# Performance work log

Measured on AMD Instinct MI355X. Metric: run time of the kernel, lower is better.

Reference implementation:

```python
import jax, jax.numpy as jnp
import numpy as np
from jax import lax

EPS = 1e-5
DIM = 96      # channels = dim
KS = 96       # kernel_size == H == W
GROUPS = 8
BATCH = 4
FFN_F = 2.66

# relative index table: emb[c, i, j] = rel[c, i - j + KS - 1]
_REL_IDX = (np.arange(KS)[:, None] - np.arange(KS)[None, :] + KS - 1).reshape(-1)


def _bn(x, g, b, ax):
    """BatchNorm (training-mode batch statistics) over all axes except `ax`."""
    axes = tuple(i for i in range(x.ndim) if i != ax)
    m = x.mean(axes, keepdims=True)
    v = x.var(axes, keepdims=True)
    sh = [1] * x.ndim
    sh[ax] = -1
    return (x - m) / jnp.sqrt(v + EPS) * g.reshape(sh) + b.reshape(sh)


def _ln(x, w, b):
    """WithBias LayerNorm over channel dim of NCHW (per-pixel over C)."""
    m = x.mean(1, keepdims=True)
    v = x.var(1, keepdims=True)
    return (x - m) / jnp.sqrt(v + EPS) * w[None, :, None, None] + b[None, :, None, None]


def _axial(x, wqkv, gq, bq, rel, gs, bs, go, bo, width):
    # x: (N, C, H, W)
    xp = x.transpose(0, 2, 1, 3) if width else x.transpose(0, 3, 1, 2)
    N, Wd, C, L = xp.shape
    gp = C // GROUPS  # group_planes
    xb = xp.reshape(N * Wd, C, L)
    qkv = _bn(jnp.einsum('oc,bcl->bol', wqkv, xb), gq, bq, 1)
    qkv = qkv.reshape(N * Wd, GROUPS, 2 * gp, L)
    q, k, v = qkv[:, :, :gp // 2], qkv[:, :, gp // 2:gp], qkv[:, :, gp:]
    emb = rel[:, _REL_IDX].reshape(2 * gp, L, L)
    qe, ke, ve = emb[:gp // 2], emb[gp // 2:gp], emb[gp:]
    qk = jnp.einsum('bgci,bgcj->bgij', q, k)
    qr = jnp.einsum('bgci,cij->bgij', q, qe)
    kr = jnp.einsum('bgci,cij->bgij', k, ke).transpose(0, 1, 3, 2)
    sim = _bn(jnp.concatenate([qk, qr, kr], 1), gs, bs, 1)
    sim = sim.reshape(N * Wd, 3, GROUPS, L, L).sum(1)
    sim = jax.nn.softmax(sim, axis=3)
    sv = jnp.einsum('bgij,bgcj->bgci', sim, v)
    sve = jnp.einsum('bgij,cij->bgci', sim, ve)
    out = _bn(jnp.concatenate([sv, sve], -1).reshape(N * Wd, 2 * C, L), go, bo, 1)
    out = out.reshape(N, Wd, C, 2, L).sum(3)
    return out.transpose(0, 2, 1, 3) if width else out.transpose(0, 2, 3, 1)


def _ffn(x, win, wdw, wout):
    h = jnp.einsum('oc,bchw->bohw', win, x)
    h = lax.conv_general_dilated(h, wdw, (1, 1), 'SAME',
                                 dimension_numbers=('NCHW', 'OIHW', 'NCHW'),
                                 feature_group_count=h.shape[1])
    x1, x2 = jnp.split(h, 2, axis=1)
    return jnp.einsum('oc,bchw->bohw', wout, jax.nn.gelu(x1, approximate=False) * x2)


def setup_inputs() -> dict:
    key = jax.random.key(0)
    ks = jax.random.split(key, 8)
    dim, gp = DIM, DIM // GROUPS
    hid = int(dim * FFN_F)
    f = jax.random.normal
    d = {'x': f(ks[0], (BATCH, dim, KS, KS), jnp.float32)}
    d['ln1_w'] = jnp.ones(dim); d['ln1_b'] = jnp.zeros(dim)
    for p, i in (('h_', 1), ('w_', 2)):
        k1, k2 = jax.random.split(ks[i])
        d[p + 'wqkv'] = f(k1, (2 * dim, dim), jnp.float32) * float(np.sqrt(1.0 / dim))
        d[p + 'gqkv'] = jnp.ones(2 * dim); d[p + 'bqkv'] = jnp.zeros(2 * dim)
        d[p + 'rel'] = f(k2, (2 * gp, 2 * KS - 1), jnp.float32) * float(np.sqrt(1.0 / gp))
        d[p + 'gsim'] = jnp.ones(3 * GROUPS); d[p + 'bsim'] = jnp.zeros(3 * GROUPS)
        d[p + 'gout'] = jnp.ones(2 * dim); d[p + 'bout'] = jnp.zeros(2 * dim)
    d['ln2_w'] = jnp.ones(dim); d['ln2_b'] = jnp.zeros(dim)
    d['ffn_win'] = f(ks[3], (2 * hid, dim), jnp.float32) * float(np.sqrt(1.0 / dim))
    d['ffn_wdw'] = f(ks[4], (2 * hid, 1, 3, 3), jnp.float32) * 0.1
    d['ffn_wout'] = f(ks[5], (dim, hid), jnp.float32) * float(np.sqrt(1.0 / hid))
    return d


def reference(x, ln1_w, ln1_b,
              h_wqkv, h_gqkv, h_bqkv, h_rel, h_gsim, h_bsim, h_gout, h_bout,
              w_wqkv, w_gqkv, w_bqkv, w_rel, w_gsim, w_bsim, w_gout, w_bout,
              ln2_w, ln2_b, ffn_win, ffn_wdw, ffn_wout):
    y = _ln(x, ln1_w, ln1_b)
    y = _axial(y, h_wqkv, h_gqkv, h_bqkv, h_rel, h_gsim, h_bsim, h_gout, h_bout, False)
    y = _axial(y, w_wqkv, w_gqkv, w_bqkv, w_rel, w_gsim, w_bsim, w_gout, w_bout, True)
    x = x + y
    x = x + _ffn(_ln(x, ln2_w, ln2_b), ffn_win, ffn_wdw, ffn_wout)
    return x
```

## Files before the change

kernel.cpp:

```cpp
#include <hip/hip_runtime.h>
#include <hip/hip_bf16.h>
#include <math.h>

using bf16 = __hip_bfloat16;

#define NB 4
#define C_ 96
#define NPIX 36864
#define IMG 9216
#define CH_ST 9216
#define N_ST 884736
#define HID 255
#define EPSF 1e-5f
#define TOT 3538944

__global__ __launch_bounds__(256) void ln_kernel(const float* __restrict__ X,
                                                 float* __restrict__ Y,
                                                 const float* __restrict__ w,
                                                 const float* __restrict__ b) {
  int pix = blockIdx.x * 256 + threadIdx.x;
  if (pix >= NPIX) return;
  int n = pix / IMG, p = pix % IMG;
  const float* xp = X + (long)n * N_ST + p;
  float s = 0.f, sq = 0.f;
  for (int c = 0; c < C_; c++) { float v = xp[c * CH_ST]; s += v; sq += v * v; }
  float m = s * (1.f / C_);
  float var = fmaxf(sq * (1.f / C_) - m * m, 0.f);
  float r = rsqrtf(var + EPSF);
  float* yp = Y + (long)n * N_ST + p;
  for (int c = 0; c < C_; c++)
    yp[c * CH_ST] = (xp[c * CH_ST] - m) * r * w[c] + b[c];
}

__global__ void trans_kernel(const float* __restrict__ Y0, float* __restrict__ Y0C) {
  __shared__ float T[32][33];
  int nc = blockIdx.z; int n = nc / C_, c = nc % C_;
  int h0 = blockIdx.x * 32, w0 = blockIdx.y * 32;
  int tx = threadIdx.x, ty = threadIdx.y;
  const float* src = Y0 + (long)n * N_ST + (long)c * CH_ST;
  for (int r = 0; r < 4; r++)
    T[ty + 8 * r][tx] = src[(h0 + ty + 8 * r) * 96 + w0 + tx];
  __syncthreads();
  float* dst = Y0C + (long)c * NPIX + (long)n * IMG;
  for (int r = 0; r < 4; r++)
    dst[(w0 + ty + 8 * r) * 96 + h0 + tx] = T[tx][ty + 8 * r];
}

template<int TM, int TN, int EPI>
__global__ __launch_bounds__(256) void gemm_kernel(
    const float* __restrict__ A, const float* __restrict__ B,
    float* __restrict__ Cout, int M, int K, int NperZ,
    long bCstride, long bZstride, int batch,
    const float* __restrict__ X1, float* __restrict__ OutF) {
  constexpr int NT = TN / 16;
  constexpr int RT = TM / 16;
  __shared__ float As[32][TM];
  __shared__ float Bs[32][TN + 4];
  const int tx = threadIdx.x, ty = threadIdx.y;
  const int tid = ty * 16 + tx;
  const int m0 = blockIdx.y * TM;
  const int q0 = blockIdx.x * TN;
  const int z  = blockIdx.z;
  const float* Bz = B + (long)z * bZstride;
  float acc[RT][NT];
  #pragma unroll
  for (int a = 0; a < RT; a++)
    #pragma unroll
    for (int b = 0; b < NT; b++) acc[a][b] = 0.f;

  for (int kk = 0; kk < K; kk += 32) {
    #pragma unroll
    for (int it = 0; it < (32 * TM) / 256; it++) {
      int i = tid + it * 256;
      int c = i / TM, r = i % TM;
      int mm = m0 + r, kc = kk + c;
      As[c][r] = (mm < M && kc < K) ? A[(long)mm * K + kc] : 0.f;
    }
    #pragma unroll
    for (int it = 0; it < (32 * TN) / 256; it++) {
      int i = tid + it * 256;
      int c = i / TN, q = i % TN;
      int kc = kk + c;
      Bs[c][q] = (kc < K) ? Bz[(long)kc * bCstride + q0 + q] : 0.f;
    }
    __syncthreads();
    for (int kc = 0; kc < 32; kc++) {
      float av[RT];
      if constexpr (RT % 4 == 0) {
        #pragma unroll
        for (int u = 0; u < RT / 4; u++) {
          float4 a4 = *(const float4*)&As[kc][ty * RT + 4 * u];
          av[4 * u] = a4.x; av[4 * u + 1] = a4.y; av[4 * u + 2] = a4.z; av[4 * u + 3] = a4.w;
        }
      } else {
        #pragma unroll
        for (int u = 0; u < RT / 2; u++) {
          float2 a2 = *(const float2*)&As[kc][ty * RT + 2 * u];
          av[2 * u] = a2.x; av[2 * u + 1] = a2.y;
        }
      }
      float bv[NT];
      #pragma unroll
      for (int v4 = 0; v4 < NT / 4; v4++) {
        float4 b4 = *(const float4*)&Bs[kc][v4 * 64 + tx * 4];
        bv[v4 * 4] = b4.x; bv[v4 * 4 + 1] = b4.y; bv[v4 * 4 + 2] = b4.z; bv[v4 * 4 + 3] = b4.w;
      }
      #pragma unroll
      for (int a = 0; a < RT; a++)
        #pragma unroll
        for (int b = 0; b < NT; b++)
          acc[a][b] = fmaf(av[a], bv[b], acc[a][b]);
    }
    __syncthreads();
  }
  const long oStride = (long)NperZ * gridDim.z;
  if (EPI == 0) {
    #pragma unroll
    for (int a = 0; a < RT; a++) {
      int mm = m0 + ty * RT + a;
      if (mm < M) {
        float* dst = Cout + (long)mm * oStride + (long)z * NperZ + q0;
        #pragma unroll
        for (int v4 = 0; v4 < NT / 4; v4++)
          *(float4*)(dst + v4 * 64 + tx * 4) =
              make_float4(acc[a][v4 * 4], acc[a][v4 * 4 + 1],
                          acc[a][v4 * 4 + 2], acc[a][v4 * 4 + 3]);
      }
    }
  } else {
    #pragma unroll
    for (int a = 0; a < RT; a++) {
      int mm = m0 + ty * RT + a;
      if (mm < M) {
        #pragma unroll
        for (int v4 = 0; v4 < NT / 4; v4++) {
          int Q = q0 + v4 * 64 + tx * 4;
          int n = batch + z + Q / IMG, p = Q % IMG;
          long base = (long)n * N_ST + (long)mm * CH_ST + p;
          #pragma unroll
          for (int b = 0; b < 4; b++)
            OutF[base + b] = acc[a][v4 * 4 + b] + X1[base + b];
        }
      }
    }
  }
}

__global__ __launch_bounds__(1024) void rowstat_kernel(const float* __restrict__ D,
                                                       const float* __restrict__ g,
                                                       const float* __restrict__ b,
                                                       float2* __restrict__ aff) {
  int o = blockIdx.x;
  const float4* p = (const float4*)(D + (long)o * NPIX);
  float s = 0.f, sq = 0.f;
  for (int i = threadIdx.x; i < NPIX / 4; i += 1024) {
    float4 v = p[i];
    s  += v.x + v.y + v.z + v.w;
    sq += v.x * v.x + v.y * v.y + v.z * v.z + v.w * v.w;
  }
  for (int off = 32; off; off >>= 1) { s += __shfl_down(s, off); sq += __shfl_down(sq, off); }
  __shared__ float ss[16], ssq[16];
  int wv = threadIdx.x >> 6, lane = threadIdx.x & 63;
  if (lane == 0) { ss[wv] = s; ssq[wv] = sq; }
  __syncthreads();
  if (threadIdx.x == 0) {
    float S = 0.f, SQ = 0.f;
    #pragma unroll
    for (int i = 0; i < 16; i++) { S += ss[i]; SQ += ssq[i]; }
    float m = S / (float)NPIX;
    float var = fmaxf(SQ / (float)NPIX - m * m, 0.f);
    float sc = g[o] * rsqrtf(var + EPSF);
    aff[o] = make_float2(sc, b[o] - m * sc);
  }
}

__global__ void relstat_kernel(const float* __restrict__ relp, float* __restrict__ tbl) {
  int i = threadIdx.x;
  if (i >= 96) return;
  int side = blockIdx.x / 27, row = blockIdx.x % 27;
  const float* base = relp + side * 6 * 191;
  float* T = tbl + side * 27 * 96;
  if (row < 6) {
    float s = 0.f;
    for (int d = 0; d < 96; d++) s += base[row * 191 + i + d];
    T[row * 96 + i] = s;
  } else {
    int p = row - 6, c = 0;
    while (p >= 6 - c) { p -= 6 - c; c++; }
    int c2 = c + p;
    float s = 0.f;
    for (int d = 0; d < 96; d++) s += base[c * 191 + i + d] * base[c2 * 191 + i + d];
    T[576 + (row - 6) * 96 + i] = s;
  }
}

__global__ __launch_bounds__(256) void simstat2_kernel(const float* __restrict__ QKV,
                                                       const float2* __restrict__ aff,
                                                       const float* __restrict__ tbl,
                                                       float* __restrict__ stats) {
  int g = blockIdx.x & 7, chunk = blockIdx.x >> 3;
  int bbg = threadIdx.x >> 5, lane = threadIdx.x & 31;
  int bb = chunk * 8 + bbg;
  const float* Aq = tbl;
  const float* Wq = tbl + 6 * 96;
  const float* Ak = tbl + 27 * 96;
  const float* Wk = tbl + 27 * 96 + 6 * 96;
  float Sq[6] = {}, Sk[6] = {}, Gq[21] = {}, Gk[21] = {};
  float lq = 0.f, lsq = 0.f, lk = 0.f, lsk = 0.f;
  #pragma unroll
  for (int ii = 0; ii < 3; ii++) {
    int i = lane + 32 * ii;
    float qv[6], kv[6];
    #pragma unroll
    for (int c = 0; c < 6; c++) {
      int oq = g * 24 + c, ok = g * 24 + 6 + c;
      float2 a = aff[oq], b2 = aff[ok];
      qv[c] = QKV[(long)oq * NPIX + bb * 96 + i] * a.x + a.y;
      kv[c] = QKV[(long)ok * NPIX + bb * 96 + i] * b2.x + b2.y;
      Sq[c] += qv[c]; Sk[c] += kv[c];
      lq = fmaf(qv[c], Aq[c * 96 + i], lq);
      lk = fmaf(kv[c], Ak[c * 96 + i], lk);
    }
    int p = 0;
    #pragma unroll
    for (int c = 0; c < 6; c++)
      #pragma unroll
      for (int c2 = c; c2 < 6; c2++, p++) {
        float f = (c == c2) ? 1.f : 2.f;
        float pq = qv[c] * qv[c2], pk = kv[c] * kv[c2];
        Gq[p] += pq; Gk[p] += pk;
        lsq = fmaf(pq * f, Wq[p * 96 + i], lsq);
        lsk = fmaf(pk * f, Wk[p * 96 + i], lsk);
      }
  }
  #pragma unroll
  for (int off = 16; off; off >>= 1) {
    #pragma unroll
    for (int c = 0; c < 6; c++) { Sq[c] += __shfl_down(Sq[c], off, 32); Sk[c] += __shfl_down(Sk[c], off, 32); }
    #pragma unroll
    for (int p = 0; p < 21; p++) { Gq[p] += __shfl_down(Gq[p], off, 32); Gk[p] += __shfl_down(Gk[p], off, 32); }
    lq += __shfl_down(lq, off, 32);  lsq += __shfl_down(lsq, off, 32);
    lk += __shfl_down(lk, off, 32);  lsk += __shfl_down(lsk, off, 32);
  }
  __shared__ float red[6];
  if (threadIdx.x < 6) red[threadIdx.x] = 0.f;
  __syncthreads();
  if (lane == 0) {
    float sqk = 0.f, sqk2 = 0.f;
    #pragma unroll
    for (int c = 0; c < 6; c++) sqk += Sq[c] * Sk[c];
    int p = 0;
    #pragma unroll
    for (int c = 0; c < 6; c++)
      #pragma unroll
      for (int c2 = c; c2 < 6; c2++, p++)
        sqk2 += ((c == c2) ? 1.f : 2.f) * Gq[p] * Gk[p];
    atomicAdd(&red[0], sqk); atomicAdd(&red[3], sqk2);
    atomicAdd(&red[1], lq);  atomicAdd(&red[4], lsq);
    atomicAdd(&red[2], lk);  atomicAdd(&red[5], lsk);
  }
  __syncthreads();
  if (threadIdx.x < 3) {
    atomicAdd(&stats[(threadIdx.x * 8 + g) * 2 + 0], red[threadIdx.x]);
    atomicAdd(&stats[(threadIdx.x * 8 + g) * 2 + 1], red[threadIdx.x + 3]);
  }
}

__global__ void simfin_kernel(const float* __restrict__ stats,
                              const float* __restrict__ gsim,
                              float* __restrict__ scale) {
  int t = threadIdx.x;
  if (t < 24) {
    float cnt = 384.f * 9216.f;
    float m = stats[t * 2] / cnt;
    float var = fmaxf(stats[t * 2 + 1] / cnt - m * m, 0.f);
    scale[t] = gsim[t] * rsqrtf(var + EPSF);
  }
}

__global__ __launch_bounds__(256) void attn_kernel(const float* __restrict__ QKV,
                                                   const float2* __restrict__ aff,
                                                   const float* __restrict__ relp,
                                                   const float* __restrict__ sscale,
                                                   float* __restrict__ OutPre) {
  int blk = blockIdx.x;
  int bb = blk / 24, rem = blk % 24;
  int g = rem / 3, iq = rem % 3;
  int i0 = iq * 32;
  __shared__ float qI[6][32];
  __shared__ float kF[6][96];
  __shared__ float vF[12][96];
  __shared__ float rl[24][191];
  __shared__ float P[32][100];
  __shared__ float rinv[32];
  int tid = threadIdx.x;
  float s0 = sscale[g], s1 = sscale[8 + g], s2 = sscale[16 + g];
  for (int i = tid; i < 6 * 32; i += 256) {
    int c = i >> 5, l = i & 31;
    int o = g * 24 + c; float2 a = aff[o];
    qI[c][l] = QKV[(long)o * NPIX + bb * 96 + i0 + l] * a.x + a.y;
  }
  for (int i = tid; i < 6 * 96; i += 256) {
    int c = i / 96, l = i % 96;
    int o = g * 24 + 6 + c; float2 a = aff[o];
    kF[c][l] = QKV[(long)o * NPIX + bb * 96 + l] * a.x + a.y;
  }
  for (int i = tid; i < 12 * 96; i += 256) {
    int c = i / 96, l = i % 96;
    int o = g * 24 + 12 + c; float2 a = aff[o];
    vF[c][l] = QKV[(long)o * NPIX + bb * 96 + l] * a.x + a.y;
  }
  for (int i = tid; i < 24 * 191; i += 256) {
    int r = i / 191;
    float sc = (r < 6) ? s1 : ((r < 12) ? s2 : 1.f);
    (&rl[0][0])[i] = relp[i] * sc;
  }
  __syncthreads();
  int hw = tid >> 5, l32 = tid & 31;
  {
    int til = hw * 4;
    int ti = i0 + til;
    int tj = l32 * 3;
    int d0 = ti - tj + 93;
    int e0 = tj - ti + 92;
    float ap[4][3] = {};
    #pragma unroll
    for (int c = 0; c < 6; c++) {
      float4 q4 = *(const float4*)&qI[c][til];
      float qv[4] = {q4.x, q4.y, q4.z, q4.w};
      float kv[3], kv0[3], rq[6], rk[6];
      #pragma unroll
      for (int j = 0; j < 3; j++) { kv[j] = kF[c][tj + j]; kv0[j] = s0 * kv[j]; }
      #pragma unroll
      for (int u = 0; u < 6; u++) { rq[u] = rl[c][d0 + u]; rk[u] = rl[6 + c][e0 + u]; }
      #pragma unroll
      for (int ii = 0; ii < 4; ii++)
        #pragma unroll
        for (int jj = 0; jj < 3; jj++) {
          ap[ii][jj] = fmaf(qv[ii], kv0[jj], ap[ii][jj]);
          ap[ii][jj] = fmaf(qv[ii], rq[ii - jj + 2], ap[ii][jj]);
          ap[ii][jj] = fmaf(kv[jj], rk[jj - ii + 3], ap[ii][jj]);
        }
    }
    #pragma unroll
    for (int ii = 0; ii < 4; ii++)
      #pragma unroll
      for (int jj = 0; jj < 3; jj++)
        P[til + ii][l32 * 3 + jj] = ap[ii][jj];
  }
  __syncthreads();
  for (int r = hw; r < 32; r += 8) {
    float v0 = P[r][l32], v1 = P[r][l32 + 32], v2 = P[r][l32 + 64];
    float mx = fmaxf(v0, fmaxf(v1, v2));
    #pragma unroll
    for (int off = 16; off; off >>= 1) mx = fmaxf(mx, __shfl_xor(mx, off, 32));
    float e0 = __expf(v0 - mx), e1 = __expf(v1 - mx), e2 = __expf(v2 - mx);
    P[r][l32] = e0; P[r][l32 + 32] = e1; P[r][l32 + 64] = e2;
    float s = e0 + e1 + e2;
    #pragma unroll
    for (int off = 16; off; off >>= 1) s += __shfl_xor(s, off, 32);
    if (l32 == 0) rinv[r] = 1.f / s;
  }
  __syncthreads();
  {
    int orr0 = hw * 3;
    float acc3[3] = {};
    for (int jq = 0; jq < 24; jq++) {
      int j0 = jq * 4;
      float4 pv = *(const float4*)&P[l32][j0];
      #pragma unroll
      for (int u = 0; u < 3; u++) {
        int orr = orr0 + u, cc = orr >> 1;
        if ((orr & 1) == 0) {
          float4 vv = *(const float4*)&vF[cc][j0];
          acc3[u] += pv.x * vv.x + pv.y * vv.y + pv.z * vv.z + pv.w * vv.w;
        } else {
          const float* rv = rl[12 + cc];
          int bse = (i0 + l32) - j0 + 92;
          float f0 = rv[bse], f1 = rv[bse + 1], f2 = rv[bse + 2], f3 = rv[bse + 3];
          acc3[u] += pv.w * f0 + pv.z * f1 + pv.y * f2 + pv.x * f3;
        }
      }
    }
    #pragma unroll
    for (int u = 0; u < 3; u++)
      OutPre[(long)(g * 24 + orr0 + u) * NPIX + bb * 96 + i0 + l32] = acc3[u] * rinv[l32];
  }
}

__global__ void apply1_kernel(const float* __restrict__ OutPre,
                              const float2* __restrict__ aff,
                              float* __restrict__ Y1) {
  __shared__ float T[32][33];
  int z = blockIdx.z; int n = z / C_, cf = z % C_;
  int h0 = blockIdx.x * 32, w0 = blockIdx.y * 32;
  int tx = threadIdx.x, ty = threadIdx.y;
  float2 a0 = aff[2 * cf], a1 = aff[2 * cf + 1];
  const float* r0 = OutPre + (long)(2 * cf) * NPIX + (long)n * IMG;
  const float* r1 = OutPre + (long)(2 * cf + 1) * NPIX + (long)n * IMG;
  for (int r = 0; r < 4; r++) {
    int w = w0 + ty + 8 * r;
    int idx = w * 96 + h0 + tx;
    T[ty + 8 * r][tx] = (r0[idx] * a0.x + a0.y) + (r1[idx] * a1.x + a1.y);
  }
  __syncthreads();
  float* dst = Y1 + (long)n * N_ST + (long)cf * CH_ST;
  for (int r = 0; r < 4; r++)
    dst[(h0 + ty + 8 * r) * 96 + w0 + tx] = T[tx][ty + 8 * r];
}

__global__ __launch_bounds__(256) void apply2_kernel(const float* __restrict__ OutPre,
                                                     const float2* __restrict__ aff,
                                                     const float* __restrict__ X,
                                                     float* __restrict__ X1out) {
  int idx = blockIdx.x * 256 + threadIdx.x;
  if (idx >= TOT) return;
  int n = idx / N_ST;
  int rem = idx % N_ST;
  int cf = rem / CH_ST;
  int p = rem % CH_ST;
  long off = (long)n * IMG + p;
  float2 a0 = aff[2 * cf], a1 = aff[2 * cf + 1];
  float v = OutPre[(long)(2 * cf) * NPIX + off] * a0.x + a0.y
          + OutPre[(long)(2 * cf + 1) * NPIX + off] * a1.x + a1.y
          + X[idx];
  X1out[idx] = v;
}

__global__ __launch_bounds__(256) void dwglu_kernel(const float* __restrict__ H,
                                                    const float* __restrict__ Wdw,
                                                    float* __restrict__ Gout) {
  int idx = blockIdx.x * 256 + threadIdx.x;
  if (idx >= HID * IMG) return;
  int c = idx / IMG;
  int p = idx % IMG, y = p / 96, x = p % 96;
  const float* h1 = H + (long)c * IMG;
  const float* h2 = H + (long)(c + HID) * IMG;
  const float* w1 = Wdw + c * 9;
  const float* w2 = Wdw + (c + HID) * 9;
  float acc1 = 0.f, acc2 = 0.f;
  #pragma unroll
  for (int dy = -1; dy <= 1; dy++) {
    int yy = y + dy; if (yy < 0 || yy >= 96) continue;
    #pragma unroll
    for (int dx = -1; dx <= 1; dx++) {
      int xx = x + dx; if (xx < 0 || xx >= 96) continue;
      int wi = (dy + 1) * 3 + dx + 1;
      acc1 = fmaf(h1[yy * 96 + xx], w1[wi], acc1);
      acc2 = fmaf(h2[yy * 96 + xx], w2[wi], acc2);
    }
  }
  float ge = 0.5f * acc1 * (1.f + erff(acc1 * 0.70710678118654752f));
  Gout[idx] = ge * acc2;
}

extern "C" void kernel_launch(void* const* d_in, const int* in_sizes, int n_in,
                              void* d_out, int out_size, void* d_ws, size_t ws_size,
                              hipStream_t stream) {
  const float* x       = (const float*)d_in[0];
  const float* ln1w    = (const float*)d_in[1];
  const float* ln1b    = (const float*)d_in[2];
  const float* h_wqkv  = (const float*)d_in[3];
  const float* h_gqkv  = (const float*)d_in[4];
  const float* h_bqkv  = (const float*)d_in[5];
  const float* h_rel   = (const float*)d_in[6];
  const float* h_gsim  = (const float*)d_in[7];
  const float* h_gout  = (const float*)d_in[9];
  const float* h_bout  = (const float*)d_in[10];
  const float* w_wqkv  = (const float*)d_in[11];
  const float* w_gqkv  = (const float*)d_in[12];
  const float* w_bqkv  = (const float*)d_in[13];
  const float* w_rel   = (const float*)d_in[14];
  const float* w_gsim  = (const float*)d_in[15];
  const float* w_gout  = (const float*)d_in[17];
  const float* w_bout  = (const float*)d_in[18];
  const float* ln2w    = (const float*)d_in[19];
  const float* ln2b    = (const float*)d_in[20];
  const float* ffn_win = (const float*)d_in[21];
  const float* ffn_wdw = (const float*)d_in[22];
  const float* ffn_wout= (const float*)d_in[23];
  float* out = (float*)d_out;

  float* ws = (float*)d_ws;
  float* P = ws;
  float* Q = ws + 3538944;
  float* R = ws + 7077888;
  float* S = ws + 14155776;
  float* Gall = R;
  float* Hbuf = ws + 16478208;
  float* stats = ws + 21233664;
  const size_t need_bytes = (21233664ull + 8192ull) * 4ull;
  if (ws_size < need_bytes) return;

  float2* qkv_aff = (float2*)stats;
  float2* out_aff = (float2*)(stats + 384);
  float*  sim_st  = stats + 768;
  float*  sim_sc  = stats + 864;
  float*  tbl     = stats + 1024;

  hipMemsetAsync(sim_st, 0, 96 * sizeof(float), stream);

  dim3 b256(256), b1616(16, 16), b328(32, 8);

  ln_kernel<<<144, b256, 0, stream>>>(x, P, ln1w, ln1b);
  trans_kernel<<<dim3(3, 3, 384), b328, 0, stream>>>(P, Q);

  gemm_kernel<96, 128, 0><<<dim3(288, 2, 1), b1616, 0, stream>>>(h_wqkv, Q, R,
      192, 96, 36864, 36864L, 0L, 0, nullptr, nullptr);
  rowstat_kernel<<<192, 1024, 0, stream>>>(R, h_gqkv, h_bqkv, qkv_aff);
  relstat_kernel<<<54, 96, 0, stream>>>(h_rel, tbl);
  simstat2_kernel<<<384, b256, 0, stream>>>(R, qkv_aff, tbl, sim_st);
  simfin_kernel<<<1, 32, 0, stream>>>(sim_st, h_gsim, sim_sc);
  attn_kernel<<<9216, b256, 0, stream>>>(R, qkv_aff, h_rel, sim_sc, S);
  rowstat_kernel<<<192, 1024, 0, stream>>>(S, h_gout, h_bout, out_aff);
  apply1_kernel<<<dim3(3, 3, 384), b328, 0, stream>>>(S, out_aff, P);

  gemm_kernel<96, 128, 0><<<dim3(72, 2, 4), b1616, 0, stream>>>(w_wqkv, P, R,
      192, 96, 9216, 9216L, 884736L, 0, nullptr, nullptr);
  rowstat_kernel<<<192, 1024, 0, stream>>>(R, w_gqkv, w_bqkv, qkv_aff);
  relstat_kernel<<<54, 96, 0, stream>>>(w_rel, tbl);
  simstat2_kernel<<<384, b256, 0, stream>>>(R, qkv_aff, tbl, sim_st + 48);
  simfin_kernel<<<1, 32, 0, stream>>>(sim_st + 48, w_gsim, sim_sc + 24);
  attn_kernel<<<9216, b256, 0, stream>>>(R, qkv_aff, w_rel, sim_sc + 24, S);
  rowstat_kernel<<<192, 1024, 0, stream>>>(S, w_gout, w_bout, out_aff);
  apply2_kernel<<<13824, b256, 0, stream>>>(S, out_aff, x, P);

  ln_kernel<<<144, b256, 0, stream>>>(P, Q, ln2w, ln2b);
  for (int n = 0; n < NB; n++) {
    gemm_kernel<128, 64, 0><<<dim3(144, 4, 1), b1616, 0, stream>>>(ffn_win, Q + (long)n * N_ST, Hbuf,
        510, 96, 9216, 9216L, 0L, 0, nullptr, nullptr);
    dwglu_kernel<<<9180, b256, 0, stream>>>(Hbuf, ffn_wdw, Gall + (long)n * 2350080);
  }
  gemm_kernel<96, 64, 1><<<dim3(144, 1, 4), b1616, 0, stream>>>(ffn_wout, Gall, nullptr,
      96, 255, 9216, 9216L, 2350080L, 0, P, out);
}
```

Baseline: 941.7 us.

## Process all query tiles per block in axial attention to reuse staged K/V/rel

Each attention block now handles one (batch-row, group) pair and loops over the three 32-row query tiles, so the K, V and scaled relative-embedding tables are loaded into shared memory once instead of three times. The global loads of Q/K/V and the rel table are also vectorised to float4. The grid shrinks threefold, which cuts redundant staging traffic but leaves fewer blocks for latency hiding and adds extra barriers inside the loop.

```diff
diff --git a/kernel.cpp b/kernel.cpp
--- a/kernel.cpp
+++ b/kernel.cpp
@@ -284,107 +284,118 @@
                                                    const float* __restrict__ sscale,
                                                    float* __restrict__ OutPre) {
   int blk = blockIdx.x;
-  int bb = blk / 24, rem = blk % 24;
-  int g = rem / 3, iq = rem % 3;
-  int i0 = iq * 32;
-  __shared__ float qI[6][32];
+  int bb = blk >> 3, g = blk & 7;
+  __shared__ float qF[6][96];
   __shared__ float kF[6][96];
   __shared__ float vF[12][96];
-  __shared__ float rl[24][191];
+  __shared__ float rl[24 * 191];
   __shared__ float P[32][100];
-  __shared__ float rinv[32];
   int tid = threadIdx.x;
   float s0 = sscale[g], s1 = sscale[8 + g], s2 = sscale[16 + g];
-  for (int i = tid; i < 6 * 32; i += 256) {
-    int c = i >> 5, l = i & 31;
-    int o = g * 24 + c; float2 a = aff[o];
-    qI[c][l] = QKV[(long)o * NPIX + bb * 96 + i0 + l] * a.x + a.y;
-  }
-  for (int i = tid; i < 6 * 96; i += 256) {
-    int c = i / 96, l = i % 96;
-    int o = g * 24 + 6 + c; float2 a = aff[o];
-    kF[c][l] = QKV[(long)o * NPIX + bb * 96 + l] * a.x + a.y;
-  }
-  for (int i = tid; i < 12 * 96; i += 256) {
-    int c = i / 96, l = i % 96;
-    int o = g * 24 + 12 + c; float2 a = aff[o];
-    vF[c][l] = QKV[(long)o * NPIX + bb * 96 + l] * a.x + a.y;
-  }
-  for (int i = tid; i < 24 * 191; i += 256) {
-    int r = i / 191;
-    float sc = (r < 6) ? s1 : ((r < 12) ? s2 : 1.f);
-    (&rl[0][0])[i] = relp[i] * sc;
+  for (int i = tid; i < 288; i += 256) {
+    int half = i / 144, r = i % 144;
+    int c = r / 24, qd = r % 24;
+    int o = g * 24 + half * 6 + c;
+    float2 a = aff[o];
+    float4 v = *(const float4*)(QKV + (long)o * NPIX + bb * 96 + qd * 4);
+    float4 w = make_float4(v.x * a.x + a.y, v.y * a.x + a.y,
+                           v.z * a.x + a.y, v.w * a.x + a.y);
+    if (half == 0) *(float4*)&qF[c][qd * 4] = w;
+    else           *(float4*)&kF[c][qd * 4] = w;
+  }
+  for (int i = tid; i < 288; i += 256) {
+    int c = i / 24, qd = i % 24;
+    int o = g * 24 + 12 + c;
+    float2 a = aff[o];
+    float4 v = *(const float4*)(QKV + (long)o * NPIX + bb * 96 + qd * 4);
+    *(float4*)&vF[c][qd * 4] = make_float4(v.x * a.x + a.y, v.y * a.x + a.y,
+                                           v.z * a.x + a.y, v.w * a.x + a.y);
+  }
+  for (int i = tid; i < 1146; i += 256) {
+    int e = i * 4;
+    float4 v = *(const float4*)(relp + e);
+    float4 w;
+    w.x = v.x * ((e + 0) < 1146 ? s1 : (e + 0) < 2292 ? s2 : 1.f);
+    w.y = v.y * ((e + 1) < 1146 ? s1 : (e + 1) < 2292 ? s2 : 1.f);
+    w.z = v.z * ((e + 2) < 1146 ? s1 : (e + 2) < 2292 ? s2 : 1.f);
+    w.w = v.w * ((e + 3) < 1146 ? s1 : (e + 3) < 2292 ? s2 : 1.f);
+    *(float4*)&rl[e] = w;
   }
   __syncthreads();
   int hw = tid >> 5, l32 = tid & 31;
-  {
-    int til = hw * 4;
-    int ti = i0 + til;
-    int tj = l32 * 3;
-    int d0 = ti - tj + 93;
-    int e0 = tj - ti + 92;
-    float ap[4][3] = {};
-    #pragma unroll
-    for (int c = 0; c < 6; c++) {
-      float4 q4 = *(const float4*)&qI[c][til];
-      float qv[4] = {q4.x, q4.y, q4.z, q4.w};
-      float kv[3], kv0[3], rq[6], rk[6];
-      #pragma unroll
-      for (int j = 0; j < 3; j++) { kv[j] = kF[c][tj + j]; kv0[j] = s0 * kv[j]; }
-      #pragma unroll
-      for (int u = 0; u < 6; u++) { rq[u] = rl[c][d0 + u]; rk[u] = rl[6 + c][e0 + u]; }
+  for (int iq = 0; iq < 3; iq++) {
+    int i0 = iq * 32;
+    {
+      int til = hw * 4;
+      int ti = i0 + til;
+      int tj = l32 * 3;
+      int d0 = ti - tj + 93;
+      int e0 = tj - ti + 92;
+      float ap[4][3] = {};
+      #pragma unroll
+      for (int c = 0; c < 6; c++) {
+        float4 q4 = *(const float4*)&qF[c][ti];
+        float qv[4] = {q4.x, q4.y, q4.z, q4.w};
+        float kv[3], kv0[3], rq[6], rk[6];
+        #pragma unroll
+        for (int j = 0; j < 3; j++) { kv[j] = kF[c][tj + j]; kv0[j] = s0 * kv[j]; }
+        #pragma unroll
+        for (int u = 0; u < 6; u++) { rq[u] = rl[c * 191 + d0 + u]; rk[u] = rl[(6 + c) * 191 + e0 + u]; }
+        #pragma unroll
+        for (int ii = 0; ii < 4; ii++)
+          #pragma unroll
+          for (int jj = 0; jj < 3; jj++) {
+            ap[ii][jj] = fmaf(qv[ii], kv0[jj], ap[ii][jj]);
+            ap[ii][jj] = fmaf(qv[ii], rq[ii - jj + 2], ap[ii][jj]);
+            ap[ii][jj] = fmaf(kv[jj], rk[jj - ii + 3], ap[ii][jj]);
+          }
+      }
       #pragma unroll
       for (int ii = 0; ii < 4; ii++)
         #pragma unroll
-        for (int jj = 0; jj < 3; jj++) {
-          ap[ii][jj] = fmaf(qv[ii], kv0[jj], ap[ii][jj]);
-          ap[ii][jj] = fmaf(qv[ii], rq[ii - jj + 2], ap[ii][jj]);
-          ap[ii][jj] = fmaf(kv[jj], rk[jj - ii + 3], ap[ii][jj]);
+        for (int jj = 0; jj < 3; jj++)
+          P[til + ii][l32 * 3 + jj] = ap[ii][jj];
+    }
+    __syncthreads();
+    for (int r = hw; r < 32; r += 8) {
+      float v0 = P[r][l32], v1 = P[r][l32 + 32], v2 = P[r][l32 + 64];
+      float mx = fmaxf(v0, fmaxf(v1, v2));
+      #pragma unroll
+      for (int off = 16; off; off >>= 1) mx = fmaxf(mx, __shfl_xor(mx, off, 32));
+      float e0 = __expf(v0 - mx), e1 = __expf(v1 - mx), e2 = __expf(v2 - mx);
+      P[r][l32] = e0; P[r][l32 + 32] = e1; P[r][l32 + 64] = e2;
+      float s = e0 + e1 + e2;
+      #pragma unroll
+      for (int off = 16; off; off >>= 1) s += __shfl_xor(s, off, 32);
+      if (l32 == 0) P[r][96] = 1.f / s;
+    }
+    __syncthreads();
+    {
+      int orr0 = hw * 3;
+      float acc3[3] = {};
+      for (int jq = 0; jq < 24; jq++) {
+        int j0 = jq * 4;
+        float4 pv = *(const float4*)&P[l32][j0];
+        #pragma unroll
+        for (int u = 0; u < 3; u++) {
+          int orr = orr0 + u, cc = orr >> 1;
+          if ((orr & 1) == 0) {
+            float4 vv = *(const float4*)&vF[cc][j0];
+            acc3[u] += pv.x * vv.x + pv.y * vv.y + pv.z * vv.z + pv.w * vv.w;
+          } else {
+            const float* rv = &rl[(12 + cc) * 191];
+            int bse = (i0 + l32) - j0 + 92;
+            float f0 = rv[bse], f1 = rv[bse + 1], f2 = rv[bse + 2], f3 = rv[bse + 3];
+            acc3[u] += pv.w * f0 + pv.z * f1 + pv.y * f2 + pv.x * f3;
+          }
         }
-    }
-    #pragma unroll
-    for (int ii = 0; ii < 4; ii++)
-      #pragma unroll
-      for (int jj = 0; jj < 3; jj++)
-        P[til + ii][l32 * 3 + jj] = ap[ii][jj];
-  }
-  __syncthreads();
-  for (int r = hw; r < 32; r += 8) {
-    float v0 = P[r][l32], v1 = P[r][l32 + 32], v2 = P[r][l32 + 64];
-    float mx = fmaxf(v0, fmaxf(v1, v2));
-    #pragma unroll
-    for (int off = 16; off; off >>= 1) mx = fmaxf(mx, __shfl_xor(mx, off, 32));
-    float e0 = __expf(v0 - mx), e1 = __expf(v1 - mx), e2 = __expf(v2 - mx);
-    P[r][l32] = e0; P[r][l32 + 32] = e1; P[r][l32 + 64] = e2;
-    float s = e0 + e1 + e2;
-    #pragma unroll
-    for (int off = 16; off; off >>= 1) s += __shfl_xor(s, off, 32);
-    if (l32 == 0) rinv[r] = 1.f / s;
-  }
-  __syncthreads();
-  {
-    int orr0 = hw * 3;
-    float acc3[3] = {};
-    for (int jq = 0; jq < 24; jq++) {
-      int j0 = jq * 4;
-      float4 pv = *(const float4*)&P[l32][j0];
-      #pragma unroll
-      for (int u = 0; u < 3; u++) {
-        int orr = orr0 + u, cc = orr >> 1;
-        if ((orr & 1) == 0) {
-          float4 vv = *(const float4*)&vF[cc][j0];
-          acc3[u] += pv.x * vv.x + pv.y * vv.y + pv.z * vv.z + pv.w * vv.w;
-        } else {
-          const float* rv = rl[12 + cc];
-          int bse = (i0 + l32) - j0 + 92;
-          float f0 = rv[bse], f1 = rv[bse + 1], f2 = rv[bse + 2], f3 = rv[bse + 3];
-          acc3[u] += pv.w * f0 + pv.z * f1 + pv.y * f2 + pv.x * f3;
-        }
-      }
-    }
-    #pragma unroll
-    for (int u = 0; u < 3; u++)
-      OutPre[(long)(g * 24 + orr0 + u) * NPIX + bb * 96 + i0 + l32] = acc3[u] * rinv[l32];
+      }
+      float ri = P[l32][96];
+      #pragma unroll
+      for (int u = 0; u < 3; u++)
+        OutPre[(long)(g * 24 + orr0 + u) * NPIX + bb * 96 + i0 + l32] = acc3[u] * ri;
+    }
+    __syncthreads();
   }
 }
 
@@ -511,7 +522,7 @@
   relstat_kernel<<<54, 96, 0, stream>>>(h_rel, tbl);
   simstat2_kernel<<<384, b256, 0, stream>>>(R, qkv_aff, tbl, sim_st);
   simfin_kernel<<<1, 32, 0, stream>>>(sim_st, h_gsim, sim_sc);
-  attn_kernel<<<9216, b256, 0, stream>>>(R, qkv_aff, h_rel, sim_sc, S);
+  attn_kernel<<<3072, b256, 0, stream>>>(R, qkv_aff, h_rel, sim_sc, S);
   rowstat_kernel<<<192, 1024, 0, stream>>>(S, h_gout, h_bout, out_aff);
   apply1_kernel<<<dim3(3, 3, 384), b328, 0, stream>>>(S, out_aff, P);
 
@@ -521,7 +532,7 @@
   relstat_kernel<<<54, 96, 0, stream>>>(w_rel, tbl);
   simstat2_kernel<<<384, b256, 0, stream>>>(R, qkv_aff, tbl, sim_st + 48);
   simfin_kernel<<<1, 32, 0, stream>>>(sim_st + 48, w_gsim, sim_sc + 24);
-  attn_kernel<<<9216, b256, 0, stream>>>(R, qkv_aff, w_rel, sim_sc + 24, S);
+  attn_kernel<<<3072, b256, 0, stream>>>(R, qkv_aff, w_rel, sim_sc + 24, S);
   rowstat_kernel<<<192, 1024, 0, stream>>>(S, w_gout, w_bout, out_aff);
   apply2_kernel<<<13824, b256, 0, stream>>>(S, out_aff, x, P);
 
```

New measurement: 950.1 us. Within noise of the previous version (+0.9%).
